# Kernel tuning notes

Measured on AMD Instinct MI355X. Metric: run time of the kernel, lower is better.

Reference implementation:

```python
import jax, jax.numpy as jnp
import numpy as np

B, F, V, D = 16384, 16, 300000, 10


def setup_inputs() -> dict:
    key = jax.random.key(0)
    k1, k2, k3 = jax.random.split(key, 3)
    x = jax.random.randint(k1, (B, F), 0, V)
    emb = jax.random.normal(k2, (F, V, D), dtype=jnp.float32) * 0.01
    lin = jax.random.normal(k3, (V, 1), dtype=jnp.float32) * 0.01
    return {"x": x, "emb": emb, "lin": lin}


def reference(x, emb, lin):
    # x: [B, F] int ids; emb: [F, V, D] per-field embedding tables; lin: [V, 1]
    F_, V_, D_ = emb.shape
    Bsz = x.shape[0]
    # pair indices (i < j), same order as the nested python loops (i outer, j inner)
    ii, jj = jnp.triu_indices(F_, k=1)  # each [P], P = F*(F-1)/2
    # a[p, b] = emb[j_p][ x[b, i_p] ]  (table j indexed by field-i id)
    a = emb[jj[:, None], x[:, ii].T]   # [P, B, D]
    # b[p, b] = emb[i_p][ x[b, j_p] ]
    b = emb[ii[:, None], x[:, jj].T]   # [P, B, D]
    pair = (a * b).transpose(1, 0, 2).reshape(Bsz, -1)  # [B, P*D]
    # self embeddings: emb[i][ x[:, i] ] for each field i, concatenated
    self_e = emb[jnp.arange(F_)[None, :], x].reshape(Bsz, -1)  # [B, F*D]
    # linear term: lin[x].view(-1, F)
    lin_e = lin[x][..., 0]  # [B, F]
    return jnp.concatenate([pair, self_e, lin_e], axis=1)  # [B, P*D + F*D + F]
```

## Files before the change

kernel.cpp:

```cpp
#include <hip/hip_runtime.h>

#define Bsz   16384
#define Fn    16
#define Vn    300000
#define Dn    10
#define NPAIR 120
#define OUT_ROW 1376
#define ROWS_PER_BLOCK 4

__device__ const unsigned char PAIR_IJ[NPAIR] = {
    1,2,3,4,5,6,7,8,9,10,11,12,13,14,15,
    18,19,20,21,22,23,24,25,26,27,28,29,30,31,
    35,36,37,38,39,40,41,42,43,44,45,46,47,
    52,53,54,55,56,57,58,59,60,61,62,63,
    69,70,71,72,73,74,75,76,77,78,79,
    86,87,88,89,90,91,92,93,94,95,
    103,104,105,106,107,108,109,110,111,
    120,121,122,123,124,125,126,127,
    137,138,139,140,141,142,143,
    154,155,156,157,158,159,
    171,172,173,174,175,
    188,189,190,191,
    205,206,207,
    222,223,
    239
};

__global__ __launch_bounds__(256) void ffm_kernel(
    const int*   __restrict__ x,
    const float* __restrict__ emb,
    const float* __restrict__ lin,
    float*       __restrict__ out)
{
    __shared__ float tile[ROWS_PER_BLOCK][Fn][Fn][Dn];

    const int w    = threadIdx.x >> 6;
    const int lane = threadIdx.x & 63;
    const int row  = blockIdx.x * ROWS_PER_BLOCK + w;

    const int xv = x[row * Fn + (lane & 15)];

    const float lv = lin[xv];

    float2 buf[4][5];
    #pragma unroll
    for (int t = 0; t < 4; ++t) {
        const int q = lane + 64 * t;
        const int f = q >> 4;
        const int g = q & 15;
        const int idx = __shfl(xv, f);
        const float2* src = (const float2*)(emb + ((size_t)g * Vn + (size_t)idx) * Dn);
        #pragma unroll
        for (int c = 0; c < 5; ++c) buf[t][c] = src[c];
    }
    #pragma unroll
    for (int t = 0; t < 4; ++t) {
        const int q = lane + 64 * t;
        const int f = q >> 4;
        const int g = q & 15;
        float2* dst = (float2*)&tile[w][f][g][0];
        #pragma unroll
        for (int c = 0; c < 5; ++c) dst[c] = buf[t][c];
    }
    __syncthreads();

    float* orow = out + (size_t)row * OUT_ROW;
    for (int k = lane; k < 1360; k += 64) {
        float val;
        if (k < 1200) {
            const int p = k / 10;
            const int d = k - p * 10;
            const int ij = PAIR_IJ[p];
            const int i = ij >> 4, j = ij & 15;
            val = tile[w][i][j][d] * tile[w][j][i][d];
        } else {
            const int t2 = k - 1200;
            const int f = t2 / 10;
            const int d = t2 - f * 10;
            val = tile[w][f][f][d];
        }
        orow[k] = val;
    }

    if (lane < Fn) {
        orow[1360 + lane] = lv;
    }
}

extern "C" void kernel_launch(void* const* d_in, const int* in_sizes, int n_in,
                              void* d_out, int out_size, void* d_ws, size_t ws_size,
                              hipStream_t stream) {
    const int*   x   = (const int*)d_in[0];
    const float* emb = (const float*)d_in[1];
    const float* lin = (const float*)d_in[2];
    float*       out = (float*)d_out;

    const int blocks = Bsz / ROWS_PER_BLOCK;
    ffm_kernel<<<blocks, 256, 0, stream>>>(x, emb, lin, out);
}
```

Baseline: 355.6 us.

## Gather embeddings directly per output element instead of staging in LDS

Removes the shared-memory tile and barrier. Each lane now computes its output elements by loading the two needed embedding scalars straight from global memory with shuffled indices. The self-embedding tail and the linear terms are merged into one final 32-lane store, and launch bounds request higher occupancy. The trade is scalar, uncoalesced 4-byte loads in place of float2 vector loads into LDS, with each element fetched twice, relying on cache hits and more waves in flight to hide latency.

Measured after the change: 343.0 us. 1.04x faster.

```diff
diff --git a/kernel.cpp b/kernel.cpp
--- a/kernel.cpp
+++ b/kernel.cpp
@@ -4,11 +4,10 @@
 #define Fn    16
 #define Vn    300000
 #define Dn    10
-#define NPAIR 120
 #define OUT_ROW 1376
 #define ROWS_PER_BLOCK 4
 
-__device__ const unsigned char PAIR_IJ[NPAIR] = {
+__device__ const unsigned char PAIR_IJ[120] = {
     1,2,3,4,5,6,7,8,9,10,11,12,13,14,15,
     18,19,20,21,22,23,24,25,26,27,28,29,30,31,
     35,36,37,38,39,40,41,42,43,44,45,46,47,
@@ -26,64 +25,46 @@
     239
 };
 
-__global__ __launch_bounds__(256) void ffm_kernel(
+__global__ __launch_bounds__(256, 8) void ffm_kernel(
     const int*   __restrict__ x,
     const float* __restrict__ emb,
     const float* __restrict__ lin,
     float*       __restrict__ out)
 {
-    __shared__ float tile[ROWS_PER_BLOCK][Fn][Fn][Dn];
-
-    const int w    = threadIdx.x >> 6;
+    const int wave = threadIdx.x >> 6;
     const int lane = threadIdx.x & 63;
-    const int row  = blockIdx.x * ROWS_PER_BLOCK + w;
+    const int row  = blockIdx.x * ROWS_PER_BLOCK + wave;
 
     const int xv = x[row * Fn + (lane & 15)];
+    float* orow = out + (size_t)row * OUT_ROW;
 
     const float lv = lin[xv];
+    const int t2   = 144 + (lane & 15);
+    const int f_ep = t2 / 10;
+    const int d_ep = t2 - f_ep * 10;
+    const int xf_ep = __shfl(xv, f_ep);
+    const float self_ep = emb[(unsigned)(f_ep * Vn + xf_ep) * 10u + d_ep];
 
-    float2 buf[4][5];
-    #pragma unroll
-    for (int t = 0; t < 4; ++t) {
-        const int q = lane + 64 * t;
-        const int f = q >> 4;
-        const int g = q & 15;
-        const int idx = __shfl(xv, f);
-        const float2* src = (const float2*)(emb + ((size_t)g * Vn + (size_t)idx) * Dn);
-        #pragma unroll
-        for (int c = 0; c < 5; ++c) buf[t][c] = src[c];
-    }
-    #pragma unroll
-    for (int t = 0; t < 4; ++t) {
-        const int q = lane + 64 * t;
-        const int f = q >> 4;
-        const int g = q & 15;
-        float2* dst = (float2*)&tile[w][f][g][0];
-        #pragma unroll
-        for (int c = 0; c < 5; ++c) dst[c] = buf[t][c];
-    }
-    __syncthreads();
-
-    float* orow = out + (size_t)row * OUT_ROW;
-    for (int k = lane; k < 1360; k += 64) {
-        float val;
-        if (k < 1200) {
-            const int p = k / 10;
-            const int d = k - p * 10;
-            const int ij = PAIR_IJ[p];
-            const int i = ij >> 4, j = ij & 15;
-            val = tile[w][i][j][d] * tile[w][j][i][d];
-        } else {
-            const int t2 = k - 1200;
-            const int f = t2 / 10;
-            const int d = t2 - f * 10;
-            val = tile[w][f][f][d];
-        }
-        orow[k] = val;
+    #pragma unroll 3
+    for (int it = 0; it < 21; ++it) {
+        const int k = lane + (it << 6);
+        const int p = k / 10;
+        const int d = k - p * 10;
+        const bool isPair = k < 1200;
+        const int pc = isPair ? p : 0;
+        const int ij = PAIR_IJ[pc];
+        const int f  = p - 120;
+        const int i  = isPair ? (ij >> 4) : f;
+        const int j  = isPair ? (ij & 15) : f;
+        const int xi = __shfl(xv, i);
+        const int xj = __shfl(xv, j);
+        const float A = emb[(unsigned)(j * Vn + xi) * 10u + d];
+        const float B = emb[(unsigned)(i * Vn + xj) * 10u + d];
+        orow[k] = isPair ? A * B : A;
     }
 
-    if (lane < Fn) {
-        orow[1360 + lane] = lv;
+    if (lane < 32) {
+        orow[1344 + lane] = (lane < 16) ? self_ep : lv;
     }
 }
 
```
